# Kernel optimization log

Hardware: AMD Instinct MI355X
Metric: run time of the kernel (lower is better)

## Reference

```python
import jax, jax.numpy as jnp
import numpy as np

D_IN = 128
HID = 32
HEADS = 8
OUT = 16
N = 50000
E = 400000
NEG_SLOPE = 0.2


def setup_inputs() -> dict:
    key = jax.random.key(0)
    ks = jax.random.split(key, 12)
    s = lambda k, sh: jax.random.normal(k, sh, dtype=jnp.float32) * 0.05
    return {
        "x": jax.random.normal(ks[0], (N, D_IN), dtype=jnp.float32),
        "edge_index": jax.random.randint(ks[1], (2, E), 0, N, dtype=jnp.int64),
        # conv_1: GATv2, heads=8, concat=True
        "W1l": s(ks[2], (D_IN, HEADS * HID)),
        "W1r": s(ks[3], (D_IN, HEADS * HID)),
        "att1": s(ks[4], (HEADS, HID)),
        "b1": jnp.zeros((HEADS * HID,), dtype=jnp.float32),
        # conv_2: GATv2, heads=1, concat=False
        "W2l": s(ks[5], (HEADS * HID, HID)),
        "W2r": s(ks[6], (HEADS * HID, HID)),
        "att2": s(ks[7], (1, HID)),
        "b2": jnp.zeros((HID,), dtype=jnp.float32),
        # final linear
        "Wlin": s(ks[8], (HID, OUT)),
        "blin": jnp.zeros((OUT,), dtype=jnp.float32),
    }


def _gatv2(x, src, dst, Wl, Wr, att, bias, n_nodes):
    heads, ch = att.shape
    xl = (x @ Wl).reshape(n_nodes, heads, ch)   # source-side transform
    xr = (x @ Wr).reshape(n_nodes, heads, ch)   # target-side transform
    # per-edge GATv2 score: a^T leaky_relu(xl_i + xr_j)
    e = jax.nn.leaky_relu(xl[src] + xr[dst], NEG_SLOPE)        # [E,H,C]
    logits = jnp.einsum('ehc,hc->eh', e, att)                  # [E,H]
    # segment softmax grouped by destination node
    m = jax.ops.segment_max(logits, dst, num_segments=n_nodes)
    m = jnp.where(jnp.isfinite(m), m, 0.0)
    p = jnp.exp(logits - m[dst])
    denom = jax.ops.segment_sum(p, dst, num_segments=n_nodes)
    alpha = p / jnp.maximum(denom[dst], 1e-16)                 # [E,H]
    # scatter-sum aggregation of weighted source features
    out = jax.ops.segment_sum(alpha[:, :, None] * xl[src], dst, num_segments=n_nodes)
    return out + bias.reshape(1, heads, ch)                    # [N,H,C]


def reference(x, edge_index, W1l, W1r, att1, b1, W2l, W2r, att2, b2, Wlin, blin):
    n = x.shape[0]
    loops = jnp.arange(n, dtype=edge_index.dtype)
    ei = jnp.concatenate([edge_index, jnp.stack([loops, loops])], axis=1)  # add_self_loops=True
    src, dst = ei[0], ei[1]

    h = _gatv2(x, src, dst, W1l, W1r, att1, b1, n)   # [N,8,32]
    h = jax.nn.elu(h.reshape(n, -1))                  # concat=True; dropout=identity (eval)

    h = _gatv2(h, src, dst, W2l, W2r, att2, b2, n)   # [N,1,32]
    h = jax.nn.elu(h[:, 0, :])                        # concat=False, heads=1 -> mean == squeeze

    return h @ Wlin + blin                            # [N,16]
```

## Files before the change

### kernel.cpp

```cpp
#include <hip/hip_runtime.h>
#include <cstdint>
#include <cstddef>

#define N_NODES 50000
#define N_EDGES 400000
#define E_TOT   (N_EDGES + N_NODES)
#define D_INF   128
#define C1      256
#define HIDC    32
#define OUTC    16
#define NEG_SLOPE 0.2f
#define SCAN_B  ((N_NODES + 1023) / 1024)

typedef __bf16 bf16x8 __attribute__((ext_vector_type(8)));
typedef float  floatx4 __attribute__((ext_vector_type(4)));
typedef unsigned int uintx4 __attribute__((ext_vector_type(4)));
typedef unsigned short ushortx8 __attribute__((ext_vector_type(8)));
typedef unsigned short ushortx4 __attribute__((ext_vector_type(4)));

__device__ __forceinline__ unsigned short f2bf(float f) {
  unsigned int u = __builtin_bit_cast(unsigned int, f);
  u += 0x7FFFu + ((u >> 16) & 1u);
  return (unsigned short)(u >> 16);
}
__device__ __forceinline__ float bf2f(unsigned short u) {
  return __builtin_bit_cast(float, (unsigned int)u << 16);
}

__global__ void k_detect(const int* __restrict__ ei, int* __restrict__ flag) {
  __shared__ int s;
  if (threadIdx.x == 0) s = 0;
  __syncthreads();
  atomicOr(&s, ei[2 * threadIdx.x + 1]);
  __syncthreads();
  if (threadIdx.x == 0) *flag = (s == 0) ? 1 : 0;
}
__device__ __forceinline__ int ld_src(const int* ei, int f, int e) {
  return f ? ei[2 * e] : ei[e];
}
__device__ __forceinline__ int ld_dst(const int* ei, int f, int e) {
  return f ? ei[2 * (N_EDGES + e)] : ei[N_EDGES + e];
}

__global__ void k_transpose(const float* __restrict__ in,
                            unsigned short* __restrict__ out, int R, int C) {
  int i = blockIdx.x * 256 + threadIdx.x;
  if (i < R * C) {
    int r = i / C, c = i % C;
    out[c * R + r] = f2bf(in[i]);
  }
}

__global__ void k_deg(const int* __restrict__ ei, const int* __restrict__ flag,
                      int* __restrict__ deg) {
  int e = blockIdx.x * 256 + threadIdx.x;
  if (e < E_TOT) {
    int dst = (e < N_EDGES) ? ld_dst(ei, *flag, e) : (e - N_EDGES);
    if ((unsigned)dst < N_NODES) atomicAdd(&deg[dst], 1);
  }
}

__global__ __launch_bounds__(1024) void k_scan_blk(
    const int* __restrict__ deg, int* __restrict__ incl,
    int* __restrict__ bsum, int n) {
  __shared__ int sbuf[1024];
  const int t = threadIdx.x;
  const int i = blockIdx.x * 1024 + t;
  const int v = (i < n) ? deg[i] : 0;
  sbuf[t] = v;
  __syncthreads();
  for (int off = 1; off < 1024; off <<= 1) {
    int add = (t >= off) ? sbuf[t - off] : 0;
    __syncthreads();
    sbuf[t] += add;
    __syncthreads();
  }
  if (i < n) incl[i] = sbuf[t];
  if (t == 1023) bsum[blockIdx.x] = sbuf[1023];
}

__global__ void k_scan_top(int* __restrict__ bsum, int* __restrict__ rowptr,
                           int nb) {
  const int lane = threadIdx.x;
  const int v = (lane < nb) ? bsum[lane] : 0;
  int incl = v;
#pragma unroll
  for (int off = 1; off < 64; off <<= 1) {
    int t = __shfl_up(incl, off);
    if (lane >= off) incl += t;
  }
  if (lane < nb) bsum[lane] = incl - v;
  if (lane == 63) rowptr[N_NODES] = incl;
}

__global__ __launch_bounds__(1024) void k_scan_add(
    const int* __restrict__ deg, const int* __restrict__ incl,
    const int* __restrict__ bsum, int* __restrict__ rowptr,
    int* __restrict__ cursor, int n) {
  const int i = blockIdx.x * 1024 + threadIdx.x;
  if (i < n) {
    const int e = bsum[blockIdx.x] + incl[i] - deg[i];
    rowptr[i] = e;
    cursor[i] = e;
  }
}

__global__ void k_fill(const int* __restrict__ ei, const int* __restrict__ flag,
                       int* __restrict__ cursor, int* __restrict__ esrc) {
  int e = blockIdx.x * 256 + threadIdx.x;
  if (e < E_TOT) {
    int src, dst;
    if (e < N_EDGES) { src = ld_src(ei, *flag, e); dst = ld_dst(ei, *flag, e); }
    else             { src = dst = e - N_EDGES; }
    if ((unsigned)src < N_NODES && (unsigned)dst < N_NODES) {
      int pos = atomicAdd(&cursor[dst], 1);
      esrc[pos] = src;
    }
  }
}

__device__ __forceinline__ bf16x8 load8(const unsigned short* p) {
  uintx4 raw = *reinterpret_cast<const uintx4*>(p);
  return __builtin_bit_cast(bf16x8, raw);
}
__device__ __forceinline__ bf16x8 load8(const float* p) {
  floatx4 a = *reinterpret_cast<const floatx4*>(p);
  floatx4 b = *reinterpret_cast<const floatx4*>(p + 4);
  ushortx8 u;
#pragma unroll
  for (int i = 0; i < 4; ++i) { u[i] = f2bf(a[i]); u[4 + i] = f2bf(b[i]); }
  return __builtin_bit_cast(bf16x8, u);
}

template <int K, int NCOLS, typename AT>
__global__ __launch_bounds__(256) void k_gemm_dual(
    const AT* __restrict__ A,
    const unsigned short* __restrict__ BT0, const unsigned short* __restrict__ BT1,
    unsigned short* __restrict__ C0, unsigned short* __restrict__ C1_, int M) {
  const int wave = threadIdx.x >> 6;
  const int lane = threadIdx.x & 63;
  const int lo = lane & 15;
  const int q  = lane >> 4;
  const int unit = blockIdx.x * 4 + wave;
  const int r0 = unit * 32;
  if (r0 >= M) return;
  const bool two = (r0 + 16) < M;
  constexpr int KB = K / 32;

  bf16x8 afrag[2][KB];
#pragma unroll
  for (int kb = 0; kb < KB; ++kb)
    afrag[0][kb] = load8(A + (size_t)(r0 + lo) * K + kb * 32 + q * 8);
  if (two) {
#pragma unroll
    for (int kb = 0; kb < KB; ++kb)
      afrag[1][kb] = load8(A + (size_t)(r0 + 16 + lo) * K + kb * 32 + q * 8);
  }

#pragma unroll
  for (int o = 0; o < 2; ++o) {
    const unsigned short* BT = o ? BT1 : BT0;
    unsigned short* C = o ? C1_ : C0;
#pragma unroll
    for (int nt = 0; nt < NCOLS / 16; ++nt) {
      floatx4 acc0 = {0.f, 0.f, 0.f, 0.f};
      floatx4 acc1 = {0.f, 0.f, 0.f, 0.f};
      const unsigned short* bptr = BT + (size_t)(nt * 16 + lo) * K + q * 8;
#pragma unroll
      for (int kb = 0; kb < KB; ++kb) {
        bf16x8 b = load8(bptr + kb * 32);
        acc0 = __builtin_amdgcn_mfma_f32_16x16x32_bf16(afrag[0][kb], b, acc0, 0, 0, 0);
        if (two)
          acc1 = __builtin_amdgcn_mfma_f32_16x16x32_bf16(afrag[1][kb], b, acc1, 0, 0, 0);
      }
#pragma unroll
      for (int r = 0; r < 4; ++r) {
        C[(size_t)(r0 + q * 4 + r) * NCOLS + nt * 16 + lo] = f2bf(acc0[r]);
        if (two)
          C[(size_t)(r0 + 16 + q * 4 + r) * NCOLS + nt * 16 + lo] = f2bf(acc1[r]);
      }
    }
  }
}

__global__ __launch_bounds__(256) void k_gat1(
    const unsigned short* __restrict__ xl1, const unsigned short* __restrict__ xr1,
    const float* __restrict__ att1, const float* __restrict__ b1,
    const int* __restrict__ rowptr, const int* __restrict__ esrc,
    unsigned short* __restrict__ h1) {
  const int wave = threadIdx.x >> 6;
  const int lane = threadIdx.x & 63;
  const int dst = blockIdx.x * 4 + wave;
  if (dst >= N_NODES) return;
  const int h = lane >> 5;
  const int w = lane & 31;
  const int cb = w * 8;

  float xr[8], att[8];
  {
    ushortx8 r = *reinterpret_cast<const ushortx8*>(xr1 + (size_t)dst * C1 + cb);
    floatx4 a0 = *reinterpret_cast<const floatx4*>(att1 + cb);
    floatx4 a1 = *reinterpret_cast<const floatx4*>(att1 + cb + 4);
#pragma unroll
    for (int c = 0; c < 8; ++c) xr[c] = bf2f(r[c]);
#pragma unroll
    for (int c = 0; c < 4; ++c) { att[c] = a0[c]; att[4 + c] = a1[c]; }
  }

  const int beg = rowptr[dst], end = rowptr[dst + 1];
  const int n = end - beg;
  const int* ep = esrc + beg;

  float m = -INFINITY, l = 0.f;
  float acc[8] = {0.f, 0.f, 0.f, 0.f, 0.f, 0.f, 0.f, 0.f};

  int i = h;
  ushortx8 cur = (ushortx8)(unsigned short)0;
  if (i < n) {
    int s = ep[i];
    cur = *reinterpret_cast<const ushortx8*>(xl1 + (size_t)s * C1 + cb);
  }
  while (i < n) {
    const int inext = i + 2;
    ushortx8 nxt = cur;
    if (inext < n) {
      int s = ep[inext];
      nxt = *reinterpret_cast<const ushortx8*>(xl1 + (size_t)s * C1 + cb);
    }
    float xs[8];
#pragma unroll
    for (int c = 0; c < 8; ++c) xs[c] = bf2f(cur[c]);
    float v = 0.f;
#pragma unroll
    for (int c = 0; c < 8; ++c) {
      float e = xs[c] + xr[c];
      e = e > 0.f ? e : NEG_SLOPE * e;
      v = fmaf(e, att[c], v);
    }
    v += __shfl_xor(v, 1);
    v += __shfl_xor(v, 2);
    if (v > m) {
      const float sc = __expf(m - v);
      l *= sc;
#pragma unroll
      for (int c = 0; c < 8; ++c) acc[c] *= sc;
      m = v;
    }
    const float p = __expf(v - m);
    l += p;
#pragma unroll
    for (int c = 0; c < 8; ++c) acc[c] = fmaf(p, xs[c], acc[c]);
    cur = nxt;
    i = inext;
  }

  const float m2 = __shfl_xor(m, 32);
  const float l2 = __shfl_xor(l, 32);
  const float mm = fmaxf(m, m2);
  const float sa = (m  > -INFINITY) ? __expf(m  - mm) : 0.f;
  const float sb = (m2 > -INFINITY) ? __expf(m2 - mm) : 0.f;
  const float lt = l * sa + l2 * sb;
  float o[8];
#pragma unroll
  for (int c = 0; c < 8; ++c) {
    const float a2 = __shfl_xor(acc[c], 32);
    o[c] = acc[c] * sa + a2 * sb;
  }
  if (h == 0) {
    const float inv = 1.f / fmaxf(lt, 1e-16f);
    ushortx8 ob;
#pragma unroll
    for (int c = 0; c < 8; ++c) {
      float z = o[c] * inv + b1[cb + c];
      z = z > 0.f ? z : (__expf(z) - 1.f);
      ob[c] = f2bf(z);
    }
    *reinterpret_cast<ushortx8*>(h1 + (size_t)dst * C1 + cb) = ob;
  }
}

__global__ __launch_bounds__(256) void k_gat2(
    const unsigned short* __restrict__ xl2, const unsigned short* __restrict__ xr2,
    const float* __restrict__ att2, const float* __restrict__ b2,
    const float* __restrict__ Wlin, const float* __restrict__ blin,
    const int* __restrict__ rowptr, const int* __restrict__ esrc,
    float* __restrict__ out) {
  __shared__ float sh[4][32];
  const int wave = threadIdx.x >> 6;
  const int lane = threadIdx.x & 63;
  const int dst = blockIdx.x * 4 + wave;
  if (dst >= N_NODES) return;
  const int o8 = lane >> 3;
  const int w = lane & 7;
  const int cb = w * 4;

  float xr[4], att[4];
  {
    ushortx4 r = *reinterpret_cast<const ushortx4*>(xr2 + (size_t)dst * HIDC + cb);
    floatx4 a = *reinterpret_cast<const floatx4*>(att2 + cb);
#pragma unroll
    for (int c = 0; c < 4; ++c) { xr[c] = bf2f(r[c]); att[c] = a[c]; }
  }

  const int beg = rowptr[dst], end = rowptr[dst + 1];
  const int n = end - beg;
  const int* ep = esrc + beg;

  float m = -INFINITY, l = 0.f;
  float acc[4] = {0.f, 0.f, 0.f, 0.f};

  int i = o8;
  ushortx4 cur = (ushortx4)(unsigned short)0;
  if (i < n) {
    int s = ep[i];
    cur = *reinterpret_cast<const ushortx4*>(xl2 + (size_t)s * HIDC + cb);
  }
  while (i < n) {
    const int inext = i + 8;
    ushortx4 nxt = cur;
    if (inext < n) {
      int s = ep[inext];
      nxt = *reinterpret_cast<const ushortx4*>(xl2 + (size_t)s * HIDC + cb);
    }
    float xs[4];
#pragma unroll
    for (int c = 0; c < 4; ++c) xs[c] = bf2f(cur[c]);
    float v = 0.f;
#pragma unroll
    for (int c = 0; c < 4; ++c) {
      float e = xs[c] + xr[c];
      e = e > 0.f ? e : NEG_SLOPE * e;
      v = fmaf(e, att[c], v);
    }
    v += __shfl_xor(v, 1);
    v += __shfl_xor(v, 2);
    v += __shfl_xor(v, 4);
    if (v > m) {
      const float sc = __expf(m - v);
      l *= sc;
#pragma unroll
      for (int c = 0; c < 4; ++c) acc[c] *= sc;
      m = v;
    }
    const float p = __expf(v - m);
    l += p;
#pragma unroll
    for (int c = 0; c < 4; ++c) acc[c] = fmaf(p, xs[c], acc[c]);
    cur = nxt;
    i = inext;
  }

#pragma unroll
  for (int k = 8; k < 64; k <<= 1) {
    const float m2 = __shfl_xor(m, k);
    const float l2 = __shfl_xor(l, k);
    const float mm = fmaxf(m, m2);
    const float sa = (m  > -INFINITY) ? __expf(m  - mm) : 0.f;
    const float sb = (m2 > -INFINITY) ? __expf(m2 - mm) : 0.f;
    l = l * sa + l2 * sb;
#pragma unroll
    for (int c = 0; c < 4; ++c) {
      const float a2 = __shfl_xor(acc[c], k);
      acc[c] = acc[c] * sa + a2 * sb;
    }
    m = mm;
  }

  if (o8 == 0) {
    const float inv = 1.f / fmaxf(l, 1e-16f);
#pragma unroll
    for (int c = 0; c < 4; ++c) {
      float z = acc[c] * inv + b2[cb + c];
      z = z > 0.f ? z : (__expf(z) - 1.f);
      sh[wave][cb + c] = z;
    }
  }
  if (lane < OUTC) {
    float o = blin[lane];
#pragma unroll
    for (int k = 0; k < 32; ++k)
      o = fmaf(sh[wave][k], Wlin[k * OUTC + lane], o);
    out[(size_t)dst * OUTC + lane] = o;
  }
}

static inline int cdiv(int a, int b) { return (a + b - 1) / b; }

extern "C" void kernel_launch(void* const* d_in, const int* in_sizes, int n_in,
                              void* d_out, int out_size, void* d_ws, size_t ws_size,
                              hipStream_t stream) {
  const float* x    = (const float*)d_in[0];
  const int*   ei   = (const int*)d_in[1];
  const float* W1l  = (const float*)d_in[2];
  const float* W1r  = (const float*)d_in[3];
  const float* att1 = (const float*)d_in[4];
  const float* b1   = (const float*)d_in[5];
  const float* W2l  = (const float*)d_in[6];
  const float* W2r  = (const float*)d_in[7];
  const float* att2 = (const float*)d_in[8];
  const float* b2   = (const float*)d_in[9];
  const float* Wlin = (const float*)d_in[10];
  const float* blin = (const float*)d_in[11];
  float* out = (float*)d_out;

  char* w = (char*)d_ws;
  auto alloc = [&](size_t bytes) -> char* {
    char* p = w;
    w += (bytes + 255) & ~(size_t)255;
    return p;
  };
  char* regionA = alloc((size_t)N_NODES * C1 * 2);
  unsigned short* xl1 = (unsigned short*)regionA;
  unsigned short* xl2 = (unsigned short*)regionA;
  unsigned short* xr2 = (unsigned short*)(regionA + (size_t)N_NODES * HIDC * 2 + 256);
  unsigned short* xr1 = (unsigned short*)alloc((size_t)N_NODES * C1 * 2);
  unsigned short* h1  = xr1;
  unsigned short* W1lT = (unsigned short*)alloc((size_t)D_INF * C1 * 2);
  unsigned short* W1rT = (unsigned short*)alloc((size_t)D_INF * C1 * 2);
  unsigned short* W2lT = (unsigned short*)alloc((size_t)C1 * HIDC * 2);
  unsigned short* W2rT = (unsigned short*)alloc((size_t)C1 * HIDC * 2);
  int* rowptr = (int*)alloc((size_t)(N_NODES + 1) * 4);
  int* cursor = (int*)alloc((size_t)N_NODES * 4);
  int* deg    = (int*)alloc((size_t)N_NODES * 4);
  int* incl   = (int*)alloc((size_t)N_NODES * 4);
  int* bsum   = (int*)alloc((size_t)SCAN_B * 4);
  int* esrc   = (int*)alloc((size_t)E_TOT * 4);
  int* flag   = (int*)alloc(4);

  hipMemsetAsync(deg, 0, (size_t)N_NODES * 4, stream);
  k_detect<<<1, 64, 0, stream>>>(ei, flag);

  k_transpose<<<cdiv(D_INF * C1, 256), 256, 0, stream>>>(W1l, W1lT, D_INF, C1);
  k_transpose<<<cdiv(D_INF * C1, 256), 256, 0, stream>>>(W1r, W1rT, D_INF, C1);
  k_transpose<<<cdiv(C1 * HIDC, 256), 256, 0, stream>>>(W2l, W2lT, C1, HIDC);
  k_transpose<<<cdiv(C1 * HIDC, 256), 256, 0, stream>>>(W2r, W2rT, C1, HIDC);

  k_deg<<<cdiv(E_TOT, 256), 256, 0, stream>>>(ei, flag, deg);
  k_scan_blk<<<SCAN_B, 1024, 0, stream>>>(deg, incl, bsum, N_NODES);
  k_scan_top<<<1, 64, 0, stream>>>(bsum, rowptr, SCAN_B);
  k_scan_add<<<SCAN_B, 1024, 0, stream>>>(deg, incl, bsum, rowptr, cursor, N_NODES);
  k_fill<<<cdiv(E_TOT, 256), 256, 0, stream>>>(ei, flag, cursor, esrc);

  const int gblocks = cdiv(cdiv(N_NODES, 32), 4);

  k_gemm_dual<D_INF, C1><<<gblocks, 256, 0, stream>>>(x, W1lT, W1rT, xl1, xr1, N_NODES);

  k_gat1<<<cdiv(N_NODES, 4), 256, 0, stream>>>(xl1, xr1, att1, b1, rowptr, esrc, h1);

  k_gemm_dual<C1, HIDC><<<gblocks, 256, 0, stream>>>(h1, W2lT, W2rT, xl2, xr2, N_NODES);

  k_gat2<<<cdiv(N_NODES, 4), 256, 0, stream>>>(xl2, xr2, att2, b2, Wlin, blin,
                                               rowptr, esrc, out);
}
```

Baseline: 276.4 us.

## Drop online softmax max-tracking via leaky-relu split and per-node precompute

Rewrites leaky_relu(u) as 0.6u + 0.4|u|, so the linear part of each attention logit splits into a per-source-node term (precomputed into A1/A2 by new kernels) plus a per-destination term. The online softmax max tracking, its rescaling and the max-merge across lanes are replaced by a plain exp of a logit clamped to [-30, 30], followed by simple sum reductions. The GEMM is re-partitioned so the four waves of a block share 32 rows and each takes a subset of output column tiles; the four weight transposes become one launch. The trade is extra precompute passes and per-edge A1/A2 gathers, plus less numerical safety, since the clamped exp without max subtraction only matches the reference for moderate logit magnitudes.

```diff
diff --git a/kernel.cpp b/kernel.cpp
--- a/kernel.cpp
+++ b/kernel.cpp
@@ -9,7 +9,7 @@
 #define C1      256
 #define HIDC    32
 #define OUTC    16
-#define NEG_SLOPE 0.2f
+#define HEADS   8
 #define SCAN_B  ((N_NODES + 1023) / 1024)
 
 typedef __bf16 bf16x8 __attribute__((ext_vector_type(8)));
@@ -42,12 +42,25 @@
   return f ? ei[2 * (N_EDGES + e)] : ei[N_EDGES + e];
 }
 
-__global__ void k_transpose(const float* __restrict__ in,
-                            unsigned short* __restrict__ out, int R, int C) {
+__global__ void k_transpose_all(const float* __restrict__ W1l, const float* __restrict__ W1r,
+                                const float* __restrict__ W2l, const float* __restrict__ W2r,
+                                unsigned short* __restrict__ W1lT, unsigned short* __restrict__ W1rT,
+                                unsigned short* __restrict__ W2lT, unsigned short* __restrict__ W2rT) {
   int i = blockIdx.x * 256 + threadIdx.x;
-  if (i < R * C) {
-    int r = i / C, c = i % C;
-    out[c * R + r] = f2bf(in[i]);
+  const int S1 = D_INF * C1;
+  const int S2 = C1 * HIDC;
+  if (i < S1) {
+    int r = i / C1, c = i % C1;
+    W1lT[c * D_INF + r] = f2bf(W1l[i]);
+  } else if (i < 2 * S1) {
+    int j = i - S1; int r = j / C1, c = j % C1;
+    W1rT[c * D_INF + r] = f2bf(W1r[j]);
+  } else if (i < 2 * S1 + S2) {
+    int j = i - 2 * S1; int r = j / HIDC, c = j % HIDC;
+    W2lT[c * C1 + r] = f2bf(W2l[j]);
+  } else if (i < 2 * S1 + 2 * S2) {
+    int j = i - 2 * S1 - S2; int r = j / HIDC, c = j % HIDC;
+    W2rT[c * C1 + r] = f2bf(W2r[j]);
   }
 }
 
@@ -141,11 +154,12 @@
   const int lane = threadIdx.x & 63;
   const int lo = lane & 15;
   const int q  = lane >> 4;
-  const int unit = blockIdx.x * 4 + wave;
-  const int r0 = unit * 32;
+  const int r0 = blockIdx.x * 32;
   if (r0 >= M) return;
   const bool two = (r0 + 16) < M;
   constexpr int KB = K / 32;
+  constexpr int NT = NCOLS / 16;
+  constexpr int NTW = (NT >= 2) ? NT / 2 : 1;
 
   bf16x8 afrag[2][KB];
 #pragma unroll
@@ -157,34 +171,80 @@
       afrag[1][kb] = load8(A + (size_t)(r0 + 16 + lo) * K + kb * 32 + q * 8);
   }
 
-#pragma unroll
-  for (int o = 0; o < 2; ++o) {
-    const unsigned short* BT = o ? BT1 : BT0;
-    unsigned short* C = o ? C1_ : C0;
-#pragma unroll
-    for (int nt = 0; nt < NCOLS / 16; ++nt) {
-      floatx4 acc0 = {0.f, 0.f, 0.f, 0.f};
-      floatx4 acc1 = {0.f, 0.f, 0.f, 0.f};
-      const unsigned short* bptr = BT + (size_t)(nt * 16 + lo) * K + q * 8;
-#pragma unroll
-      for (int kb = 0; kb < KB; ++kb) {
-        bf16x8 b = load8(bptr + kb * 32);
-        acc0 = __builtin_amdgcn_mfma_f32_16x16x32_bf16(afrag[0][kb], b, acc0, 0, 0, 0);
-        if (two)
-          acc1 = __builtin_amdgcn_mfma_f32_16x16x32_bf16(afrag[1][kb], b, acc1, 0, 0, 0);
-      }
-#pragma unroll
-      for (int r = 0; r < 4; ++r) {
-        C[(size_t)(r0 + q * 4 + r) * NCOLS + nt * 16 + lo] = f2bf(acc0[r]);
-        if (two)
-          C[(size_t)(r0 + 16 + q * 4 + r) * NCOLS + nt * 16 + lo] = f2bf(acc1[r]);
-      }
-    }
-  }
+  const int out_id = wave >> 1;
+  const int ntbase = (wave & 1) * NTW;
+  const unsigned short* BT = out_id ? BT1 : BT0;
+  unsigned short* C = out_id ? C1_ : C0;
+
+#pragma unroll
+  for (int nti = 0; nti < NTW; ++nti) {
+    const int nt = ntbase + nti;
+    floatx4 acc0 = {0.f, 0.f, 0.f, 0.f};
+    floatx4 acc1 = {0.f, 0.f, 0.f, 0.f};
+    const unsigned short* bptr = BT + (size_t)(nt * 16 + lo) * K + q * 8;
+#pragma unroll
+    for (int kb = 0; kb < KB; ++kb) {
+      bf16x8 b = load8(bptr + kb * 32);
+      acc0 = __builtin_amdgcn_mfma_f32_16x16x32_bf16(afrag[0][kb], b, acc0, 0, 0, 0);
+      if (two)
+        acc1 = __builtin_amdgcn_mfma_f32_16x16x32_bf16(afrag[1][kb], b, acc1, 0, 0, 0);
+    }
+#pragma unroll
+    for (int r = 0; r < 4; ++r) {
+      C[(size_t)(r0 + q * 4 + r) * NCOLS + nt * 16 + lo] = f2bf(acc0[r]);
+      if (two)
+        C[(size_t)(r0 + 16 + q * 4 + r) * NCOLS + nt * 16 + lo] = f2bf(acc1[r]);
+    }
+  }
+}
+
+__global__ __launch_bounds__(256) void k_att_pre1(
+    const unsigned short* __restrict__ xl1, const float* __restrict__ att1,
+    float* __restrict__ A1) {
+  const int wave = threadIdx.x >> 6;
+  const int lane = threadIdx.x & 63;
+  const int h = lane >> 5;
+  const int w = lane & 31;
+  const int cb = w * 8;
+  const int node = blockIdx.x * 8 + wave * 2 + h;
+  if (node >= N_NODES) return;
+  ushortx8 r = *reinterpret_cast<const ushortx8*>(xl1 + (size_t)node * C1 + cb);
+  floatx4 a0 = *reinterpret_cast<const floatx4*>(att1 + cb);
+  floatx4 a1 = *reinterpret_cast<const floatx4*>(att1 + cb + 4);
+  float t = 0.f;
+#pragma unroll
+  for (int c = 0; c < 4; ++c) t = fmaf(bf2f(r[c]), a0[c], t);
+#pragma unroll
+  for (int c = 0; c < 4; ++c) t = fmaf(bf2f(r[4 + c]), a1[c], t);
+  t += __shfl_xor(t, 1);
+  t += __shfl_xor(t, 2);
+  if ((w & 3) == 0) A1[node * HEADS + (w >> 2)] = t;
+}
+
+__global__ __launch_bounds__(256) void k_att_pre2(
+    const unsigned short* __restrict__ xl2, const float* __restrict__ att2,
+    float* __restrict__ A2) {
+  const int wave = threadIdx.x >> 6;
+  const int lane = threadIdx.x & 63;
+  const int o8 = lane >> 3;
+  const int w = lane & 7;
+  const int cb = w * 4;
+  const int node = blockIdx.x * 32 + wave * 8 + o8;
+  if (node >= N_NODES) return;
+  ushortx4 r = *reinterpret_cast<const ushortx4*>(xl2 + (size_t)node * HIDC + cb);
+  floatx4 a = *reinterpret_cast<const floatx4*>(att2 + cb);
+  float t = 0.f;
+#pragma unroll
+  for (int c = 0; c < 4; ++c) t = fmaf(bf2f(r[c]), a[c], t);
+  t += __shfl_xor(t, 1);
+  t += __shfl_xor(t, 2);
+  t += __shfl_xor(t, 4);
+  if (w == 0) A2[node] = t;
 }
 
 __global__ __launch_bounds__(256) void k_gat1(
     const unsigned short* __restrict__ xl1, const unsigned short* __restrict__ xr1,
+    const float* __restrict__ A1,
     const float* __restrict__ att1, const float* __restrict__ b1,
     const int* __restrict__ rowptr, const int* __restrict__ esrc,
     unsigned short* __restrict__ h1) {
@@ -195,37 +255,47 @@
   const int h = lane >> 5;
   const int w = lane & 31;
   const int cb = w * 8;
+  const int head = w >> 2;
 
   float xr[8], att[8];
   {
     ushortx8 r = *reinterpret_cast<const ushortx8*>(xr1 + (size_t)dst * C1 + cb);
     floatx4 a0 = *reinterpret_cast<const floatx4*>(att1 + cb);
-    floatx4 a1 = *reinterpret_cast<const floatx4*>(att1 + cb + 4);
+    floatx4 a1v = *reinterpret_cast<const floatx4*>(att1 + cb + 4);
 #pragma unroll
     for (int c = 0; c < 8; ++c) xr[c] = bf2f(r[c]);
 #pragma unroll
-    for (int c = 0; c < 4; ++c) { att[c] = a0[c]; att[4 + c] = a1[c]; }
-  }
+    for (int c = 0; c < 4; ++c) { att[c] = a0[c]; att[4 + c] = a1v[c]; }
+  }
+  float B = 0.f;
+#pragma unroll
+  for (int c = 0; c < 8; ++c) B = fmaf(xr[c], att[c], B);
+  B += __shfl_xor(B, 1);
+  B += __shfl_xor(B, 2);
 
   const int beg = rowptr[dst], end = rowptr[dst + 1];
   const int n = end - beg;
   const int* ep = esrc + beg;
 
-  float m = -INFINITY, l = 0.f;
+  float l = 0.f;
   float acc[8] = {0.f, 0.f, 0.f, 0.f, 0.f, 0.f, 0.f, 0.f};
 
   int i = h;
   ushortx8 cur = (ushortx8)(unsigned short)0;
+  float a1 = 0.f;
   if (i < n) {
     int s = ep[i];
     cur = *reinterpret_cast<const ushortx8*>(xl1 + (size_t)s * C1 + cb);
+    a1 = A1[s * HEADS + head];
   }
   while (i < n) {
     const int inext = i + 2;
     ushortx8 nxt = cur;
+    float a1n = a1;
     if (inext < n) {
       int s = ep[inext];
       nxt = *reinterpret_cast<const ushortx8*>(xl1 + (size_t)s * C1 + cb);
+      a1n = A1[s * HEADS + head];
     }
     float xs[8];
 #pragma unroll
@@ -233,45 +303,32 @@
     float v = 0.f;
 #pragma unroll
     for (int c = 0; c < 8; ++c) {
-      float e = xs[c] + xr[c];
-      e = e > 0.f ? e : NEG_SLOPE * e;
-      v = fmaf(e, att[c], v);
+      float u = xs[c] + xr[c];
+      v = fmaf(__builtin_fabsf(u), att[c], v);
     }
     v += __shfl_xor(v, 1);
     v += __shfl_xor(v, 2);
-    if (v > m) {
-      const float sc = __expf(m - v);
-      l *= sc;
-#pragma unroll
-      for (int c = 0; c < 8; ++c) acc[c] *= sc;
-      m = v;
-    }
-    const float p = __expf(v - m);
+    float logit = fmaf(0.4f, v, 0.6f * (a1 + B));
+    logit = fminf(fmaxf(logit, -30.f), 30.f);
+    const float p = __expf(logit);
     l += p;
 #pragma unroll
     for (int c = 0; c < 8; ++c) acc[c] = fmaf(p, xs[c], acc[c]);
     cur = nxt;
+    a1 = a1n;
     i = inext;
   }
 
-  const float m2 = __shfl_xor(m, 32);
-  const float l2 = __shfl_xor(l, 32);
-  const float mm = fmaxf(m, m2);
-  const float sa = (m  > -INFINITY) ? __expf(m  - mm) : 0.f;
-  const float sb = (m2 > -INFINITY) ? __expf(m2 - mm) : 0.f;
-  const float lt = l * sa + l2 * sb;
-  float o[8];
-#pragma unroll
-  for (int c = 0; c < 8; ++c) {
-    const float a2 = __shfl_xor(acc[c], 32);
-    o[c] = acc[c] * sa + a2 * sb;
-  }
+  l += __shfl_xor(l, 32);
+#pragma unroll
+  for (int c = 0; c < 8; ++c) acc[c] += __shfl_xor(acc[c], 32);
+
   if (h == 0) {
-    const float inv = 1.f / fmaxf(lt, 1e-16f);
+    const float inv = 1.f / fmaxf(l, 1e-16f);
     ushortx8 ob;
 #pragma unroll
     for (int c = 0; c < 8; ++c) {
-      float z = o[c] * inv + b1[cb + c];
+      float z = fmaf(acc[c], inv, b1[cb + c]);
       z = z > 0.f ? z : (__expf(z) - 1.f);
       ob[c] = f2bf(z);
     }
@@ -281,6 +338,7 @@
 
 __global__ __launch_bounds__(256) void k_gat2(
     const unsigned short* __restrict__ xl2, const unsigned short* __restrict__ xr2,
+    const float* __restrict__ A2,
     const float* __restrict__ att2, const float* __restrict__ b2,
     const float* __restrict__ Wlin, const float* __restrict__ blin,
     const int* __restrict__ rowptr, const int* __restrict__ esrc,
@@ -301,26 +359,36 @@
 #pragma unroll
     for (int c = 0; c < 4; ++c) { xr[c] = bf2f(r[c]); att[c] = a[c]; }
   }
+  float B = 0.f;
+#pragma unroll
+  for (int c = 0; c < 4; ++c) B = fmaf(xr[c], att[c], B);
+  B += __shfl_xor(B, 1);
+  B += __shfl_xor(B, 2);
+  B += __shfl_xor(B, 4);
 
   const int beg = rowptr[dst], end = rowptr[dst + 1];
   const int n = end - beg;
   const int* ep = esrc + beg;
 
-  float m = -INFINITY, l = 0.f;
+  float l = 0.f;
   float acc[4] = {0.f, 0.f, 0.f, 0.f};
 
   int i = o8;
   ushortx4 cur = (ushortx4)(unsigned short)0;
+  float a2 = 0.f;
   if (i < n) {
     int s = ep[i];
     cur = *reinterpret_cast<const ushortx4*>(xl2 + (size_t)s * HIDC + cb);
+    a2 = A2[s];
   }
   while (i < n) {
     const int inext = i + 8;
     ushortx4 nxt = cur;
+    float a2n = a2;
     if (inext < n) {
       int s = ep[inext];
       nxt = *reinterpret_cast<const ushortx4*>(xl2 + (size_t)s * HIDC + cb);
+      a2n = A2[s];
     }
     float xs[4];
 #pragma unroll
@@ -328,49 +396,35 @@
     float v = 0.f;
 #pragma unroll
     for (int c = 0; c < 4; ++c) {
-      float e = xs[c] + xr[c];
-      e = e > 0.f ? e : NEG_SLOPE * e;
-      v = fmaf(e, att[c], v);
+      float u = xs[c] + xr[c];
+      v = fmaf(__builtin_fabsf(u), att[c], v);
     }
     v += __shfl_xor(v, 1);
     v += __shfl_xor(v, 2);
     v += __shfl_xor(v, 4);
-    if (v > m) {
-      const float sc = __expf(m - v);
-      l *= sc;
-#pragma unroll
-      for (int c = 0; c < 4; ++c) acc[c] *= sc;
-      m = v;
-    }
-    const float p = __expf(v - m);
+    float logit = fmaf(0.4f, v, 0.6f * (a2 + B));
+    logit = fminf(fmaxf(logit, -30.f), 30.f);
+    const float p = __expf(logit);
     l += p;
 #pragma unroll
     for (int c = 0; c < 4; ++c) acc[c] = fmaf(p, xs[c], acc[c]);
     cur = nxt;
+    a2 = a2n;
     i = inext;
   }
 
 #pragma unroll
   for (int k = 8; k < 64; k <<= 1) {
-    const float m2 = __shfl_xor(m, k);
-    const float l2 = __shfl_xor(l, k);
-    const float mm = fmaxf(m, m2);
-    const float sa = (m  > -INFINITY) ? __expf(m  - mm) : 0.f;
-    const float sb = (m2 > -INFINITY) ? __expf(m2 - mm) : 0.f;
-    l = l * sa + l2 * sb;
-#pragma unroll
-    for (int c = 0; c < 4; ++c) {
-      const float a2 = __shfl_xor(acc[c], k);
-      acc[c] = acc[c] * sa + a2 * sb;
-    }
-    m = mm;
+    l += __shfl_xor(l, k);
+#pragma unroll
+    for (int c = 0; c < 4; ++c) acc[c] += __shfl_xor(acc[c], k);
   }
 
   if (o8 == 0) {
     const float inv = 1.f / fmaxf(l, 1e-16f);
 #pragma unroll
     for (int c = 0; c < 4; ++c) {
-      float z = acc[c] * inv + b2[cb + c];
+      float z = fmaf(acc[c], inv, b2[cb + c]);
       z = z > 0.f ? z : (__expf(z) - 1.f);
       sh[wave][cb + c] = z;
     }
@@ -419,6 +473,8 @@
   unsigned short* W1rT = (unsigned short*)alloc((size_t)D_INF * C1 * 2);
   unsigned short* W2lT = (unsigned short*)alloc((size_t)C1 * HIDC * 2);
   unsigned short* W2rT = (unsigned short*)alloc((size_t)C1 * HIDC * 2);
+  float* A1   = (float*)alloc((size_t)N_NODES * HEADS * 4);
+  float* A2   = (float*)alloc((size_t)N_NODES * 4);
   int* rowptr = (int*)alloc((size_t)(N_NODES + 1) * 4);
   int* cursor = (int*)alloc((size_t)N_NODES * 4);
   int* deg    = (int*)alloc((size_t)N_NODES * 4);
@@ -430,10 +486,8 @@
   hipMemsetAsync(deg, 0, (size_t)N_NODES * 4, stream);
   k_detect<<<1, 64, 0, stream>>>(ei, flag);
 
-  k_transpose<<<cdiv(D_INF * C1, 256), 256, 0, stream>>>(W1l, W1lT, D_INF, C1);
-  k_transpose<<<cdiv(D_INF * C1, 256), 256, 0, stream>>>(W1r, W1rT, D_INF, C1);
-  k_transpose<<<cdiv(C1 * HIDC, 256), 256, 0, stream>>>(W2l, W2lT, C1, HIDC);
-  k_transpose<<<cdiv(C1 * HIDC, 256), 256, 0, stream>>>(W2r, W2rT, C1, HIDC);
+  k_transpose_all<<<cdiv(2 * D_INF * C1 + 2 * C1 * HIDC, 256), 256, 0, stream>>>(
+      W1l, W1r, W2l, W2r, W1lT, W1rT, W2lT, W2rT);
 
   k_deg<<<cdiv(E_TOT, 256), 256, 0, stream>>>(ei, flag, deg);
   k_scan_blk<<<SCAN_B, 1024, 0, stream>>>(deg, incl, bsum, N_NODES);
@@ -441,14 +495,16 @@
   k_scan_add<<<SCAN_B, 1024, 0, stream>>>(deg, incl, bsum, rowptr, cursor, N_NODES);
   k_fill<<<cdiv(E_TOT, 256), 256, 0, stream>>>(ei, flag, cursor, esrc);
 
-  const int gblocks = cdiv(cdiv(N_NODES, 32), 4);
+  const int gblocks = cdiv(N_NODES, 32);
 
   k_gemm_dual<D_INF, C1><<<gblocks, 256, 0, stream>>>(x, W1lT, W1rT, xl1, xr1, N_NODES);
-
-  k_gat1<<<cdiv(N_NODES, 4), 256, 0, stream>>>(xl1, xr1, att1, b1, rowptr, esrc, h1);
+  k_att_pre1<<<cdiv(N_NODES, 8), 256, 0, stream>>>(xl1, att1, A1);
+
+  k_gat1<<<cdiv(N_NODES, 4), 256, 0, stream>>>(xl1, xr1, A1, att1, b1, rowptr, esrc, h1);
 
   k_gemm_dual<C1, HIDC><<<gblocks, 256, 0, stream>>>(h1, W2lT, W2rT, xl2, xr2, N_NODES);
-
-  k_gat2<<<cdiv(N_NODES, 4), 256, 0, stream>>>(xl2, xr2, att2, b2, Wlin, blin,
+  k_att_pre2<<<cdiv(N_NODES, 32), 256, 0, stream>>>(xl2, att2, A2);
+
+  k_gat2<<<cdiv(N_NODES, 4), 256, 0, stream>>>(xl2, xr2, A2, att2, b2, Wlin, blin,
                                                rowptr, esrc, out);
 }
```

Result: slower. 290.9 us (+5.2%).
